# Optimization experiments

Measured on AMD Instinct MI355X. Metric: run time of the kernel, lower is better.

The kernel has to match this reference:

```python
import jax, jax.numpy as jnp
import numpy as np


def _mlp2(x, w1, b1, w2, b2):
    # two-linear MLP with tanh after each layer (Sequential(MLP, activation))
    h = jnp.tanh(x @ w1.T + b1)
    return jnp.tanh(h @ w2.T + b2)


def setup_inputs() -> dict:
    key = jax.random.key(0)
    ks = jax.random.split(key, 12)
    N, K, D, H, C = 20000, 32, 128, 128, 64
    s = 0.1
    return {
        "z": jax.random.normal(ks[0], (N, D), jnp.float32),
        "z_": jax.random.normal(ks[1], (N, K, D), jnp.float32),
        "cur_w1": s * jax.random.normal(ks[2], (H, D), jnp.float32),
        "cur_b1": jax.random.uniform(ks[3], (H,), jnp.float32, -0.1, 0.1),
        "cur_w2": s * jax.random.normal(ks[4], (H, H), jnp.float32),
        "cur_b2": jax.random.uniform(ks[5], (H,), jnp.float32, -0.1, 0.1),
        "nbr_w1": s * jax.random.normal(ks[6], (H, 2 * D), jnp.float32),
        "nbr_b1": jax.random.uniform(ks[7], (H,), jnp.float32, -0.1, 0.1),
        "nbr_w2": s * jax.random.normal(ks[8], (H, H), jnp.float32),
        "nbr_b2": jax.random.uniform(ks[9], (H,), jnp.float32, -0.1, 0.1),
        "out_w": s * jax.random.normal(ks[10], (C, 2 * H), jnp.float32),
        "out_b": jax.random.uniform(ks[11], (C,), jnp.float32, -0.1, 0.1),
    }


def reference(z, z_, cur_w1, cur_b1, cur_w2, cur_b2,
              nbr_w1, nbr_b1, nbr_w2, nbr_b2, out_w, out_b):
    N, K, D = z_.shape
    # current-node branch: [N, H]
    v = _mlp2(z, cur_w1, cur_b1, cur_w2, cur_b2)
    # neighbor branch: repeat z over K, concat with z_ -> [N, K, 2D]
    zc = jnp.concatenate([jnp.broadcast_to(z[:, None, :], (N, K, D)), z_], axis=2)
    vn = _mlp2(zc, nbr_w1, nbr_b1, nbr_w2, nbr_b2)  # [N, K, H]
    v_ = vn.sum(axis=1)  # sum-aggregate over neighbors -> [N, H]
    # output linear on concatenated features -> [N, dim_c]
    dc = jnp.concatenate([v, v_], axis=1) @ out_w.T + out_b
    return dc
```

## Files before the change

kernel.cpp:

```cpp
#include <hip/hip_runtime.h>


typedef __bf16 bf16;
typedef __bf16 bf16x2 __attribute__((ext_vector_type(2)));
typedef __bf16 bf16x8 __attribute__((ext_vector_type(8)));
typedef float  f32x4  __attribute__((ext_vector_type(4)));

#define MFMA(a, b, c) __builtin_amdgcn_mfma_f32_16x16x32_bf16((a), (b), (c), 0, 0, 0)

__device__ __forceinline__ float fast_tanh(float x) {
    float ax = __builtin_fabsf(x);
    float t  = __builtin_amdgcn_exp2f(ax * 2.885390081777927f);
    float r  = 1.0f - 2.0f * __builtin_amdgcn_rcpf(t + 1.0f);
    return __builtin_copysignf(r, x);
}

__device__ __forceinline__ bf16x8 cvt8(f32x4 a, f32x4 b) {
    bf16x8 r;
    r[0] = (bf16)a[0]; r[1] = (bf16)a[1]; r[2] = (bf16)a[2]; r[3] = (bf16)a[3];
    r[4] = (bf16)b[0]; r[5] = (bf16)b[1]; r[6] = (bf16)b[2]; r[7] = (bf16)b[3];
    return r;
}

__device__ __forceinline__ int swz128(int row, int col) {
    int c = (col >> 3) ^ (row & 15);
    return row * 256 + c * 16 + (col & 7) * 2;
}
__device__ __forceinline__ int swz256(int row, int col) {
    int c = (col >> 3) ^ (row & 15);
    return row * 512 + c * 16 + (col & 7) * 2;
}

__device__ __forceinline__ void st_pair(char* base, int off, float a, float b) {
    bf16x2 p = {(bf16)a, (bf16)b};
    *(bf16x2*)(base + off) = p;
}

__global__ __launch_bounds__(256, 2) void nbr_kernel(
    const float* __restrict__ zn, const float* __restrict__ u1,
    const float* __restrict__ w1, const float* __restrict__ w2,
    const float* __restrict__ b2,
    bf16* __restrict__ feat, int NP)
{
    __shared__ char zc_lds[2][32 * 256];
    __shared__ char h1_lds[2][32 * 256];

    const int t = threadIdx.x;
    const int wv = t >> 6, lane = t & 63, g = lane >> 4, li = lane & 15;
    const int hbase = wv * 32;

    bf16x8 w1f[2][4];
#pragma unroll
    for (int ht = 0; ht < 2; ++ht)
#pragma unroll
        for (int kb = 0; kb < 4; ++kb) {
            const float* p = w1 + (size_t)(hbase + 16*ht + li) * 256 + 128 + kb*32 + 8*g;
            w1f[ht][kb] = cvt8(*(const f32x4*)p, *(const f32x4*)(p + 4));
        }
    bf16x8 w2f[2][4];
#pragma unroll
    for (int nt = 0; nt < 2; ++nt)
#pragma unroll
        for (int kb = 0; kb < 4; ++kb) {
            const float* p = w2 + (size_t)(hbase + 16*nt + li) * 128 + kb*32 + 8*g;
            w2f[nt][kb] = cvt8(*(const f32x4*)p, *(const f32x4*)(p + 4));
        }
    float b2v[2];
#pragma unroll
    for (int nt = 0; nt < 2; ++nt) b2v[nt] = b2[hbase + 16*nt + li];

    const int sm  = t >> 3;
    const int scf = (t & 7) * 16;
    const int stride = gridDim.x;

    f32x4 r[2][4];
    f32x4 uu[2][2];
    {
        int p = blockIdx.x;
#pragma unroll
        for (int j = 0; j < 2; ++j) {
            const float* src = zn + ((size_t)(2*p + j) * 32 + sm) * 128 + scf;
#pragma unroll
            for (int q = 0; q < 4; ++q) r[j][q] = *(const f32x4*)(src + 4*q);
#pragma unroll
            for (int ht = 0; ht < 2; ++ht)
                uu[j][ht] = *(const f32x4*)(u1 + (size_t)(2*p + j) * 128 + hbase + 16*ht + 4*g);
        }
    }

    const f32x4 vzero = {0.f, 0.f, 0.f, 0.f};

    for (int p = blockIdx.x; p < NP; p += stride) {
#pragma unroll
        for (int j = 0; j < 2; ++j) {
            *(bf16x8*)(zc_lds[j] + swz128(sm, scf))     = cvt8(r[j][0], r[j][1]);
            *(bf16x8*)(zc_lds[j] + swz128(sm, scf + 8)) = cvt8(r[j][2], r[j][3]);
        }
        __syncthreads();

        const int pp = p + stride;
        if (pp < NP) {
#pragma unroll
            for (int j = 0; j < 2; ++j) {
                const float* src = zn + ((size_t)(2*pp + j) * 32 + sm) * 128 + scf;
#pragma unroll
                for (int q = 0; q < 4; ++q) r[j][q] = *(const f32x4*)(src + 4*q);
            }
        }

        f32x4 acc1[2][2][2];
#pragma unroll
        for (int j = 0; j < 2; ++j)
#pragma unroll
            for (int a = 0; a < 2; ++a)
#pragma unroll
                for (int b = 0; b < 2; ++b) acc1[j][a][b] = vzero;

        __builtin_amdgcn_s_setprio(1);
#pragma unroll
        for (int kb = 0; kb < 4; ++kb) {
            bf16x8 bz[2][2];
#pragma unroll
            for (int j = 0; j < 2; ++j)
#pragma unroll
                for (int mt = 0; mt < 2; ++mt)
                    bz[j][mt] = *(const bf16x8*)(zc_lds[j] + swz128(16*mt + li, kb*32 + 8*g));
#pragma unroll
            for (int j = 0; j < 2; ++j)
#pragma unroll
                for (int ht = 0; ht < 2; ++ht)
#pragma unroll
                    for (int mt = 0; mt < 2; ++mt)
                        acc1[j][ht][mt] = MFMA(w1f[ht][kb], bz[j][mt], acc1[j][ht][mt]);
        }
        __builtin_amdgcn_s_setprio(0);

#pragma unroll
        for (int j = 0; j < 2; ++j)
#pragma unroll
            for (int ht = 0; ht < 2; ++ht)
#pragma unroll
                for (int mt = 0; mt < 2; ++mt) {
                    float v0 = fast_tanh(acc1[j][ht][mt][0] + uu[j][ht][0]);
                    float v1 = fast_tanh(acc1[j][ht][mt][1] + uu[j][ht][1]);
                    float v2 = fast_tanh(acc1[j][ht][mt][2] + uu[j][ht][2]);
                    float v3 = fast_tanh(acc1[j][ht][mt][3] + uu[j][ht][3]);
                    int m = 16*mt + li;
                    int h = hbase + 16*ht + 4*g;
                    st_pair(h1_lds[j], swz128(m, h),     v0, v1);
                    st_pair(h1_lds[j], swz128(m, h + 2), v2, v3);
                }

        if (pp < NP) {
#pragma unroll
            for (int j = 0; j < 2; ++j)
#pragma unroll
                for (int ht = 0; ht < 2; ++ht)
                    uu[j][ht] = *(const f32x4*)(u1 + (size_t)(2*pp + j) * 128 + hbase + 16*ht + 4*g);
        }
        __syncthreads();

        f32x4 acc2[2][2][2];
#pragma unroll
        for (int j = 0; j < 2; ++j)
#pragma unroll
            for (int a = 0; a < 2; ++a)
#pragma unroll
                for (int b = 0; b < 2; ++b) acc2[j][a][b] = vzero;

        __builtin_amdgcn_s_setprio(1);
#pragma unroll
        for (int kb = 0; kb < 4; ++kb) {
            bf16x8 ah[2][2];
#pragma unroll
            for (int j = 0; j < 2; ++j)
#pragma unroll
                for (int mt = 0; mt < 2; ++mt)
                    ah[j][mt] = *(const bf16x8*)(h1_lds[j] + swz128(16*mt + li, kb*32 + 8*g));
#pragma unroll
            for (int j = 0; j < 2; ++j)
#pragma unroll
                for (int mt = 0; mt < 2; ++mt)
#pragma unroll
                    for (int nt = 0; nt < 2; ++nt)
                        acc2[j][mt][nt] = MFMA(ah[j][mt], w2f[nt][kb], acc2[j][mt][nt]);
        }
        __builtin_amdgcn_s_setprio(0);

#pragma unroll
        for (int j = 0; j < 2; ++j) {
            float s0 = 0.f, s1 = 0.f;
#pragma unroll
            for (int mt = 0; mt < 2; ++mt)
#pragma unroll
                for (int rr = 0; rr < 4; ++rr) {
                    s0 += fast_tanh(acc2[j][mt][0][rr] + b2v[0]);
                    s1 += fast_tanh(acc2[j][mt][1][rr] + b2v[1]);
                }
            s0 += __shfl_xor(s0, 16); s0 += __shfl_xor(s0, 32);
            s1 += __shfl_xor(s1, 16); s1 += __shfl_xor(s1, 32);
            if (lane < 16) {
                bf16* dst = feat + (size_t)(2*p + j) * 256 + 128 + hbase + lane;
                dst[0]  = (bf16)s0;
                dst[16] = (bf16)s1;
            }
        }
    }
}

__global__ __launch_bounds__(256, 2) void cur_kernel(
    const float* __restrict__ z,
    const float* __restrict__ w1, const float* __restrict__ b1,
    const float* __restrict__ w2, const float* __restrict__ b2,
    const float* __restrict__ nw1, const float* __restrict__ nb1,
    bf16* __restrict__ feat, float* __restrict__ u1, int N)
{
    __shared__ char z_lds[64 * 256];
    __shared__ char h1_lds[64 * 256];

    const int t = threadIdx.x;
    const int wv = t >> 6, lane = t & 63, g = lane >> 4, li = lane & 15;
    const int hbase = wv * 32;
    const int n0 = blockIdx.x * 64;

    bf16x8 w1f[2][4], w2f[2][4], wzf[2][4];
#pragma unroll
    for (int ht = 0; ht < 2; ++ht)
#pragma unroll
        for (int kb = 0; kb < 4; ++kb) {
            const float* p1 = w1 + (size_t)(hbase + 16*ht + li) * 128 + kb*32 + 8*g;
            w1f[ht][kb] = cvt8(*(const f32x4*)p1, *(const f32x4*)(p1 + 4));
            const float* p2 = w2 + (size_t)(hbase + 16*ht + li) * 128 + kb*32 + 8*g;
            w2f[ht][kb] = cvt8(*(const f32x4*)p2, *(const f32x4*)(p2 + 4));
            const float* p3 = nw1 + (size_t)(hbase + 16*ht + li) * 256 + kb*32 + 8*g;
            wzf[ht][kb] = cvt8(*(const f32x4*)p3, *(const f32x4*)(p3 + 4));
        }
    float b1v[2][4], b2v[2][4], bnv[2][4];
#pragma unroll
    for (int ht = 0; ht < 2; ++ht)
#pragma unroll
        for (int rr = 0; rr < 4; ++rr) {
            b1v[ht][rr] = b1[hbase + 16*ht + 4*g + rr];
            b2v[ht][rr] = b2[hbase + 16*ht + 4*g + rr];
            bnv[ht][rr] = nb1[hbase + 16*ht + 4*g + rr];
        }

    {
        int m = t >> 2;
        int c0 = (t & 3) * 32;
        int row = n0 + m; if (row > N - 1) row = N - 1;
        const float* src = z + (size_t)row * 128 + c0;
#pragma unroll
        for (int q = 0; q < 4; ++q) {
            f32x4 a = *(const f32x4*)(src + 8*q);
            f32x4 b = *(const f32x4*)(src + 8*q + 4);
            *(bf16x8*)(z_lds + swz128(m, c0 + 8*q)) = cvt8(a, b);
        }
    }
    __syncthreads();

    const f32x4 vzero = {0.f, 0.f, 0.f, 0.f};
    f32x4 acc1[2][4], accz[2][4];
#pragma unroll
    for (int a = 0; a < 2; ++a)
#pragma unroll
        for (int b = 0; b < 4; ++b) { acc1[a][b] = vzero; accz[a][b] = vzero; }

#pragma unroll
    for (int kb = 0; kb < 4; ++kb) {
        bf16x8 bz[4];
#pragma unroll
        for (int mt = 0; mt < 4; ++mt)
            bz[mt] = *(const bf16x8*)(z_lds + swz128(16*mt + li, kb*32 + 8*g));
#pragma unroll
        for (int ht = 0; ht < 2; ++ht)
#pragma unroll
            for (int mt = 0; mt < 4; ++mt) {
                acc1[ht][mt] = MFMA(w1f[ht][kb], bz[mt], acc1[ht][mt]);
                accz[ht][mt] = MFMA(wzf[ht][kb], bz[mt], accz[ht][mt]);
            }
    }

#pragma unroll
    for (int ht = 0; ht < 2; ++ht)
#pragma unroll
        for (int mt = 0; mt < 4; ++mt) {
            int row = n0 + 16*mt + li;
            if (row < N) {
                f32x4 v;
#pragma unroll
                for (int rr = 0; rr < 4; ++rr) v[rr] = accz[ht][mt][rr] + bnv[ht][rr];
                *(f32x4*)(u1 + (size_t)row * 128 + hbase + 16*ht + 4*g) = v;
            }
        }

#pragma unroll
    for (int ht = 0; ht < 2; ++ht)
#pragma unroll
        for (int mt = 0; mt < 4; ++mt) {
            float v0 = fast_tanh(acc1[ht][mt][0] + b1v[ht][0]);
            float v1 = fast_tanh(acc1[ht][mt][1] + b1v[ht][1]);
            float v2 = fast_tanh(acc1[ht][mt][2] + b1v[ht][2]);
            float v3 = fast_tanh(acc1[ht][mt][3] + b1v[ht][3]);
            int m = 16*mt + li;
            int h = hbase + 16*ht + 4*g;
            st_pair(h1_lds, swz128(m, h),     v0, v1);
            st_pair(h1_lds, swz128(m, h + 2), v2, v3);
        }
    __syncthreads();

    f32x4 acc2[2][4];
#pragma unroll
    for (int a = 0; a < 2; ++a)
#pragma unroll
        for (int b = 0; b < 4; ++b) acc2[a][b] = vzero;

#pragma unroll
    for (int kb = 0; kb < 4; ++kb) {
        bf16x8 bh[4];
#pragma unroll
        for (int mt = 0; mt < 4; ++mt)
            bh[mt] = *(const bf16x8*)(h1_lds + swz128(16*mt + li, kb*32 + 8*g));
#pragma unroll
        for (int ht = 0; ht < 2; ++ht)
#pragma unroll
            for (int mt = 0; mt < 4; ++mt)
                acc2[ht][mt] = MFMA(w2f[ht][kb], bh[mt], acc2[ht][mt]);
    }
#pragma unroll
    for (int ht = 0; ht < 2; ++ht)
#pragma unroll
        for (int mt = 0; mt < 4; ++mt) {
            float v0 = fast_tanh(acc2[ht][mt][0] + b2v[ht][0]);
            float v1 = fast_tanh(acc2[ht][mt][1] + b2v[ht][1]);
            float v2 = fast_tanh(acc2[ht][mt][2] + b2v[ht][2]);
            float v3 = fast_tanh(acc2[ht][mt][3] + b2v[ht][3]);
            int row = n0 + 16*mt + li;
            if (row < N) {
                int h = hbase + 16*ht + 4*g;
                bf16* dst = feat + (size_t)row * 256 + h;
                bf16x2 p01 = {(bf16)v0, (bf16)v1};
                bf16x2 p23 = {(bf16)v2, (bf16)v3};
                *(bf16x2*)(dst)     = p01;
                *(bf16x2*)(dst + 2) = p23;
            }
        }
}

__global__ __launch_bounds__(256, 2) void out_kernel(
    const bf16* __restrict__ feat,
    const float* __restrict__ ow, const float* __restrict__ ob,
    float* __restrict__ out, int N)
{
    __shared__ char f_lds[64 * 512];

    const int t = threadIdx.x, wv = t >> 6, lane = t & 63, g = lane >> 4, li = lane & 15;
    const int cbase = wv * 16;
    const int n0 = blockIdx.x * 64;

    bf16x8 owf[8];
#pragma unroll
    for (int kb = 0; kb < 8; ++kb) {
        const float* p = ow + (size_t)(cbase + li) * 256 + kb*32 + 8*g;
        owf[kb] = cvt8(*(const f32x4*)p, *(const f32x4*)(p + 4));
    }
    float obv = ob[cbase + li];

    {
        int m = t >> 2;
        int c0 = (t & 3) * 64;
        int row = n0 + m; if (row > N - 1) row = N - 1;
        const bf16* src = feat + (size_t)row * 256 + c0;
#pragma unroll
        for (int q = 0; q < 8; ++q)
            *(bf16x8*)(f_lds + swz256(m, c0 + 8*q)) = *(const bf16x8*)(src + 8*q);
    }
    __syncthreads();

    const f32x4 vzero = {0.f, 0.f, 0.f, 0.f};
    f32x4 acc[4];
#pragma unroll
    for (int a = 0; a < 4; ++a) acc[a] = vzero;

#pragma unroll
    for (int kb = 0; kb < 8; ++kb) {
        bf16x8 af[4];
#pragma unroll
        for (int mt = 0; mt < 4; ++mt)
            af[mt] = *(const bf16x8*)(f_lds + swz256(16*mt + li, kb*32 + 8*g));
#pragma unroll
        for (int mt = 0; mt < 4; ++mt)
            acc[mt] = MFMA(af[mt], owf[kb], acc[mt]);
    }
#pragma unroll
    for (int mt = 0; mt < 4; ++mt)
#pragma unroll
        for (int rr = 0; rr < 4; ++rr) {
            int row = n0 + 16*mt + 4*g + rr;
            if (row < N) out[(size_t)row * 64 + cbase + li] = acc[mt][rr] + obv;
        }
}

extern "C" void kernel_launch(void* const* d_in, const int* in_sizes, int n_in,
                              void* d_out, int out_size, void* d_ws, size_t ws_size,
                              hipStream_t stream) {
    const float* z   = (const float*)d_in[0];
    const float* zn  = (const float*)d_in[1];
    const float* cw1 = (const float*)d_in[2];
    const float* cb1 = (const float*)d_in[3];
    const float* cw2 = (const float*)d_in[4];
    const float* cb2 = (const float*)d_in[5];
    const float* nw1 = (const float*)d_in[6];
    const float* nb1 = (const float*)d_in[7];
    const float* nw2 = (const float*)d_in[8];
    const float* nb2 = (const float*)d_in[9];
    const float* ow  = (const float*)d_in[10];
    const float* ob  = (const float*)d_in[11];
    float* out = (float*)d_out;

    const int N  = in_sizes[0] / 128;
    const int NP = N / 2;
    const int nblk = (N + 63) / 64;

    bf16*  feat = (bf16*)d_ws;
    float* u1   = (float*)((char*)d_ws + (size_t)N * 256 * sizeof(bf16));

    (void)n_in; (void)out_size; (void)ws_size;

    cur_kernel<<<nblk, 256, 0, stream>>>(z, cw1, cb1, cw2, cb2, nw1, nb1, feat, u1, N);
    nbr_kernel<<<512, 256, 0, stream>>>(zn, u1, nw1, nw2, nb2, feat, NP);
    out_kernel<<<nblk, 256, 0, stream>>>(feat, ow, ob, out, N);
}
```

Baseline: 126.3 us.

## Restructure neighbor kernel to per-wave nodes with prepacked bf16 weight fragments

The neighbor MLP kernel is rewritten so each wave handles one node on its own. It loads z_ rows straight from global memory into MFMA operand fragments, with no LDS staging and no block-wide barriers. A new prep kernel packs the neighbor weights into bf16 fragment order once, and the main loop rereads those fragments from global/cache instead of keeping them in registers. Tanh is simplified by folding the 2·log2e scale into the bias, dropping abs/copysign, and summing only the reciprocal part before a final fma. The aim is to remove synchronization and LDS round-trips, at the cost of much more cache traffic for weight reads on every node.

```diff
diff --git a/kernel.cpp b/kernel.cpp
--- a/kernel.cpp
+++ b/kernel.cpp
@@ -8,11 +8,19 @@
 
 #define MFMA(a, b, c) __builtin_amdgcn_mfma_f32_16x16x32_bf16((a), (b), (c), 0, 0, 0)
 
+#define C2LOG2E 2.885390081777927f
+
 __device__ __forceinline__ float fast_tanh(float x) {
-    float ax = __builtin_fabsf(x);
-    float t  = __builtin_amdgcn_exp2f(ax * 2.885390081777927f);
-    float r  = 1.0f - 2.0f * __builtin_amdgcn_rcpf(t + 1.0f);
-    return __builtin_copysignf(r, x);
+    float t = __builtin_amdgcn_exp2f(x * C2LOG2E);
+    return 1.0f - 2.0f * __builtin_amdgcn_rcpf(t + 1.0f);
+}
+__device__ __forceinline__ float fast_tanh_fb(float acc, float uc) {
+    float t = __builtin_amdgcn_exp2f(__builtin_fmaf(acc, C2LOG2E, uc));
+    return 1.0f - 2.0f * __builtin_amdgcn_rcpf(t + 1.0f);
+}
+__device__ __forceinline__ float tanh_rpart(float acc, float uc) {
+    float t = __builtin_amdgcn_exp2f(__builtin_fmaf(acc, C2LOG2E, uc));
+    return __builtin_amdgcn_rcpf(t + 1.0f);
 }
 
 __device__ __forceinline__ bf16x8 cvt8(f32x4 a, f32x4 b) {
@@ -36,173 +44,125 @@
     *(bf16x2*)(base + off) = p;
 }
 
-__global__ __launch_bounds__(256, 2) void nbr_kernel(
-    const float* __restrict__ zn, const float* __restrict__ u1,
-    const float* __restrict__ w1, const float* __restrict__ w2,
-    const float* __restrict__ b2,
-    bf16* __restrict__ feat, int NP)
+__global__ void prep_kernel(const float* __restrict__ w1,
+                            const float* __restrict__ w2,
+                            bf16* __restrict__ pw1, bf16* __restrict__ pw2) {
+    int s = blockIdx.x * blockDim.x + threadIdx.x;
+    int lane = s & 63, tile = s >> 6;
+    int li = lane & 15, g = lane >> 4;
+    {
+        int kb = tile >> 3, ht = tile & 7;
+        const float* src = w1 + (size_t)(ht * 16 + li) * 256 + 128 + kb * 32 + g * 8;
+        bf16x8 v;
+#pragma unroll
+        for (int j = 0; j < 8; ++j) v[j] = (bf16)src[j];
+        *(bf16x8*)(pw1 + (size_t)s * 8) = v;
+    }
+    {
+        int kbh = tile >> 3, ot = tile & 7;
+        const float* src = w2 + (size_t)(ot * 16 + li) * 128 + kbh * 32 + g * 8;
+        bf16x8 v;
+#pragma unroll
+        for (int j = 0; j < 8; ++j) v[j] = (bf16)src[j];
+        *(bf16x8*)(pw2 + (size_t)s * 8) = v;
+    }
+}
+
+__global__ __launch_bounds__(128, 3) void nbr_kernel(
+    const float* __restrict__ zn, const float* __restrict__ u1f,
+    const bf16* __restrict__ pw1, const bf16* __restrict__ pw2,
+    const float* __restrict__ b2, bf16* __restrict__ feat, int N)
 {
-    __shared__ char zc_lds[2][32 * 256];
-    __shared__ char h1_lds[2][32 * 256];
-
-    const int t = threadIdx.x;
-    const int wv = t >> 6, lane = t & 63, g = lane >> 4, li = lane & 15;
-    const int hbase = wv * 32;
-
-    bf16x8 w1f[2][4];
-#pragma unroll
-    for (int ht = 0; ht < 2; ++ht)
+    __shared__ char lds[2][8192];
+
+    const int t = threadIdx.x, w = t >> 6, lane = t & 63;
+    const int li = lane & 15, g = lane >> 4;
+    char* aflds = lds[w];
+
+    float bc2[8];
+#pragma unroll
+    for (int ot = 0; ot < 8; ++ot) bc2[ot] = b2[ot * 16 + li] * C2LOG2E;
+
+    const int totWaves = gridDim.x * 2;
+    const f32x4 vzero = {0.f, 0.f, 0.f, 0.f};
+
+    for (int n = blockIdx.x * 2 + w; n < N; n += totWaves) {
+        f32x4 zf[2][4][2];
+#pragma unroll
+        for (int mt = 0; mt < 2; ++mt)
+#pragma unroll
+            for (int kb = 0; kb < 4; ++kb) {
+                const float* src = zn + ((size_t)n * 32 + 16 * mt + li) * 128 + kb * 32 + g * 8;
+                zf[mt][kb][0] = *(const f32x4*)(src);
+                zf[mt][kb][1] = *(const f32x4*)(src + 4);
+            }
+        float uc[8];
+#pragma unroll
+        for (int ht = 0; ht < 8; ++ht)
+            uc[ht] = u1f[(size_t)n * 128 + ht * 16 + li] * C2LOG2E;
+
+        f32x4 acc1[2][8];
+#pragma unroll
+        for (int mt = 0; mt < 2; ++mt)
+#pragma unroll
+            for (int ht = 0; ht < 8; ++ht) acc1[mt][ht] = vzero;
+
 #pragma unroll
         for (int kb = 0; kb < 4; ++kb) {
-            const float* p = w1 + (size_t)(hbase + 16*ht + li) * 256 + 128 + kb*32 + 8*g;
-            w1f[ht][kb] = cvt8(*(const f32x4*)p, *(const f32x4*)(p + 4));
-        }
-    bf16x8 w2f[2][4];
-#pragma unroll
-    for (int nt = 0; nt < 2; ++nt)
-#pragma unroll
-        for (int kb = 0; kb < 4; ++kb) {
-            const float* p = w2 + (size_t)(hbase + 16*nt + li) * 128 + kb*32 + 8*g;
-            w2f[nt][kb] = cvt8(*(const f32x4*)p, *(const f32x4*)(p + 4));
-        }
-    float b2v[2];
-#pragma unroll
-    for (int nt = 0; nt < 2; ++nt) b2v[nt] = b2[hbase + 16*nt + li];
-
-    const int sm  = t >> 3;
-    const int scf = (t & 7) * 16;
-    const int stride = gridDim.x;
-
-    f32x4 r[2][4];
-    f32x4 uu[2][2];
-    {
-        int p = blockIdx.x;
-#pragma unroll
-        for (int j = 0; j < 2; ++j) {
-            const float* src = zn + ((size_t)(2*p + j) * 32 + sm) * 128 + scf;
-#pragma unroll
-            for (int q = 0; q < 4; ++q) r[j][q] = *(const f32x4*)(src + 4*q);
-#pragma unroll
-            for (int ht = 0; ht < 2; ++ht)
-                uu[j][ht] = *(const f32x4*)(u1 + (size_t)(2*p + j) * 128 + hbase + 16*ht + 4*g);
-        }
-    }
-
-    const f32x4 vzero = {0.f, 0.f, 0.f, 0.f};
-
-    for (int p = blockIdx.x; p < NP; p += stride) {
-#pragma unroll
-        for (int j = 0; j < 2; ++j) {
-            *(bf16x8*)(zc_lds[j] + swz128(sm, scf))     = cvt8(r[j][0], r[j][1]);
-            *(bf16x8*)(zc_lds[j] + swz128(sm, scf + 8)) = cvt8(r[j][2], r[j][3]);
-        }
-        __syncthreads();
-
-        const int pp = p + stride;
-        if (pp < NP) {
-#pragma unroll
-            for (int j = 0; j < 2; ++j) {
-                const float* src = zn + ((size_t)(2*pp + j) * 32 + sm) * 128 + scf;
-#pragma unroll
-                for (int q = 0; q < 4; ++q) r[j][q] = *(const f32x4*)(src + 4*q);
-            }
-        }
-
-        f32x4 acc1[2][2][2];
-#pragma unroll
-        for (int j = 0; j < 2; ++j)
-#pragma unroll
-            for (int a = 0; a < 2; ++a)
-#pragma unroll
-                for (int b = 0; b < 2; ++b) acc1[j][a][b] = vzero;
-
-        __builtin_amdgcn_s_setprio(1);
-#pragma unroll
-        for (int kb = 0; kb < 4; ++kb) {
-            bf16x8 bz[2][2];
-#pragma unroll
-            for (int j = 0; j < 2; ++j)
-#pragma unroll
-                for (int mt = 0; mt < 2; ++mt)
-                    bz[j][mt] = *(const bf16x8*)(zc_lds[j] + swz128(16*mt + li, kb*32 + 8*g));
-#pragma unroll
-            for (int j = 0; j < 2; ++j)
-#pragma unroll
-                for (int ht = 0; ht < 2; ++ht)
-#pragma unroll
-                    for (int mt = 0; mt < 2; ++mt)
-                        acc1[j][ht][mt] = MFMA(w1f[ht][kb], bz[j][mt], acc1[j][ht][mt]);
-        }
-        __builtin_amdgcn_s_setprio(0);
-
-#pragma unroll
-        for (int j = 0; j < 2; ++j)
-#pragma unroll
-            for (int ht = 0; ht < 2; ++ht)
-#pragma unroll
-                for (int mt = 0; mt < 2; ++mt) {
-                    float v0 = fast_tanh(acc1[j][ht][mt][0] + uu[j][ht][0]);
-                    float v1 = fast_tanh(acc1[j][ht][mt][1] + uu[j][ht][1]);
-                    float v2 = fast_tanh(acc1[j][ht][mt][2] + uu[j][ht][2]);
-                    float v3 = fast_tanh(acc1[j][ht][mt][3] + uu[j][ht][3]);
-                    int m = 16*mt + li;
-                    int h = hbase + 16*ht + 4*g;
-                    st_pair(h1_lds[j], swz128(m, h),     v0, v1);
-                    st_pair(h1_lds[j], swz128(m, h + 2), v2, v3);
+            bf16x8 az0 = cvt8(zf[0][kb][0], zf[0][kb][1]);
+            bf16x8 az1 = cvt8(zf[1][kb][0], zf[1][kb][1]);
+#pragma unroll
+            for (int ht = 0; ht < 8; ++ht) {
+                bf16x8 wf = *(const bf16x8*)(pw1 + (size_t)((kb * 8 + ht) * 64 + lane) * 8);
+                acc1[0][ht] = MFMA(az0, wf, acc1[0][ht]);
+                acc1[1][ht] = MFMA(az1, wf, acc1[1][ht]);
+            }
+        }
+
+#pragma unroll
+        for (int mt = 0; mt < 2; ++mt)
+#pragma unroll
+            for (int ht = 0; ht < 8; ++ht) {
+                int fragbase = ((mt * 4 + (ht >> 1)) * 64 + ((ht & 1) * 2 + (li >> 3)) * 16 + g * 4) * 16
+                               + (li & 7) * 2;
+#pragma unroll
+                for (int r = 0; r < 4; ++r) {
+                    float v = fast_tanh_fb(acc1[mt][ht][r], uc[ht]);
+                    *(bf16*)(aflds + fragbase + r * 16) = (bf16)v;
                 }
-
-        if (pp < NP) {
-#pragma unroll
-            for (int j = 0; j < 2; ++j)
-#pragma unroll
-                for (int ht = 0; ht < 2; ++ht)
-                    uu[j][ht] = *(const f32x4*)(u1 + (size_t)(2*pp + j) * 128 + hbase + 16*ht + 4*g);
-        }
-        __syncthreads();
-
-        f32x4 acc2[2][2][2];
-#pragma unroll
-        for (int j = 0; j < 2; ++j)
-#pragma unroll
-            for (int a = 0; a < 2; ++a)
-#pragma unroll
-                for (int b = 0; b < 2; ++b) acc2[j][a][b] = vzero;
-
-        __builtin_amdgcn_s_setprio(1);
-#pragma unroll
-        for (int kb = 0; kb < 4; ++kb) {
-            bf16x8 ah[2][2];
-#pragma unroll
-            for (int j = 0; j < 2; ++j)
-#pragma unroll
-                for (int mt = 0; mt < 2; ++mt)
-                    ah[j][mt] = *(const bf16x8*)(h1_lds[j] + swz128(16*mt + li, kb*32 + 8*g));
-#pragma unroll
-            for (int j = 0; j < 2; ++j)
-#pragma unroll
-                for (int mt = 0; mt < 2; ++mt)
-#pragma unroll
-                    for (int nt = 0; nt < 2; ++nt)
-                        acc2[j][mt][nt] = MFMA(ah[j][mt], w2f[nt][kb], acc2[j][mt][nt]);
-        }
-        __builtin_amdgcn_s_setprio(0);
-
-#pragma unroll
-        for (int j = 0; j < 2; ++j) {
-            float s0 = 0.f, s1 = 0.f;
+            }
+
+        f32x4 acc2[2][8];
+#pragma unroll
+        for (int mt = 0; mt < 2; ++mt)
+#pragma unroll
+            for (int ot = 0; ot < 8; ++ot) acc2[mt][ot] = vzero;
+
+#pragma unroll
+        for (int kbh = 0; kbh < 4; ++kbh) {
+            bf16x8 a0 = *(const bf16x8*)(aflds + (size_t)((0 + kbh) * 64 + lane) * 16);
+            bf16x8 a1 = *(const bf16x8*)(aflds + (size_t)((4 + kbh) * 64 + lane) * 16);
+#pragma unroll
+            for (int ot = 0; ot < 8; ++ot) {
+                bf16x8 wf = *(const bf16x8*)(pw2 + (size_t)((kbh * 8 + ot) * 64 + lane) * 8);
+                acc2[0][ot] = MFMA(a0, wf, acc2[0][ot]);
+                acc2[1][ot] = MFMA(a1, wf, acc2[1][ot]);
+            }
+        }
+
+#pragma unroll
+        for (int ot = 0; ot < 8; ++ot) {
+            float s = 0.f;
 #pragma unroll
             for (int mt = 0; mt < 2; ++mt)
 #pragma unroll
-                for (int rr = 0; rr < 4; ++rr) {
-                    s0 += fast_tanh(acc2[j][mt][0][rr] + b2v[0]);
-                    s1 += fast_tanh(acc2[j][mt][1][rr] + b2v[1]);
-                }
-            s0 += __shfl_xor(s0, 16); s0 += __shfl_xor(s0, 32);
-            s1 += __shfl_xor(s1, 16); s1 += __shfl_xor(s1, 32);
+                for (int r = 0; r < 4; ++r)
+                    s += tanh_rpart(acc2[mt][ot][r], bc2[ot]);
+            s += __shfl_xor(s, 16);
+            s += __shfl_xor(s, 32);
             if (lane < 16) {
-                bf16* dst = feat + (size_t)(2*p + j) * 256 + 128 + hbase + lane;
-                dst[0]  = (bf16)s0;
-                dst[16] = (bf16)s1;
+                float v = __builtin_fmaf(-2.f, s, 32.f);
+                feat[(size_t)n * 256 + 128 + ot * 16 + li] = (bf16)v;
             }
         }
     }
@@ -418,16 +378,19 @@
     const float* ob  = (const float*)d_in[11];
     float* out = (float*)d_out;
 
-    const int N  = in_sizes[0] / 128;
-    const int NP = N / 2;
+    const int N = in_sizes[0] / 128;
     const int nblk = (N + 63) / 64;
 
-    bf16*  feat = (bf16*)d_ws;
-    float* u1   = (float*)((char*)d_ws + (size_t)N * 256 * sizeof(bf16));
+    char* ws = (char*)d_ws;
+    bf16*  feat = (bf16*)ws;
+    float* u1   = (float*)(ws + (size_t)N * 256 * sizeof(bf16));
+    bf16*  pw1  = (bf16*)(ws + (size_t)N * 256 * sizeof(bf16) + (size_t)N * 128 * sizeof(float));
+    bf16*  pw2  = pw1 + 2048 * 8;
 
     (void)n_in; (void)out_size; (void)ws_size;
 
+    prep_kernel<<<8, 256, 0, stream>>>(nw1, nw2, pw1, pw2);
     cur_kernel<<<nblk, 256, 0, stream>>>(z, cw1, cb1, cw2, cb2, nw1, nb1, feat, u1, N);
-    nbr_kernel<<<512, 256, 0, stream>>>(zn, u1, nw1, nw2, nb2, feat, NP);
+    nbr_kernel<<<1536, 128, 0, stream>>>(zn, u1, pw1, pw2, nb2, feat, N);
     out_kernel<<<nblk, 256, 0, stream>>>(feat, ow, ob, out, N);
 }
```

Result: slower. 423.6 us (+235.4%).
